# Kernel tuning notes

Hardware: AMD Instinct MI355X
Metric: run time of the kernel (lower is better)

The kernel has to match this reference:

```python
import jax, jax.numpy as jnp
import numpy as np

V, E, R, D, OUT, B = 50000, 400000, 400, 100, 200, 1024
EPS = 1e-5


def ccorr(a, b):
    # circular correlation: irfft(conj(rfft(a)) * rfft(b), n=D)
    return jnp.fft.irfft(jnp.conj(jnp.fft.rfft(a)) * jnp.fft.rfft(b), n=a.shape[-1]).astype(a.dtype)


def setup_inputs() -> dict:
    key = jax.random.key(0)
    ks = jax.random.split(key, 16)
    xav = lambda k, shp: jax.random.normal(k, shp, dtype=jnp.float32) * np.sqrt(2.0 / (shp[0] + shp[-1])) * np.sqrt(2.0)
    return {
        # graph / query (int constants)
        "edge_src": jax.random.randint(ks[0], (E,), 0, V, dtype=jnp.int32),
        "edge_dst": jax.random.randint(ks[1], (E,), 0, V, dtype=jnp.int32),
        "edge_type": jax.random.randint(ks[2], (E,), 0, R, dtype=jnp.int32),
        "head": jax.random.randint(ks[3], (B,), 0, V, dtype=jnp.int32),
        "rela": jax.random.randint(ks[4], (B,), 0, R, dtype=jnp.int32),
        "edge_norm": jax.random.uniform(ks[5], (E,), dtype=jnp.float32),
        # learned parameters
        "ent_emb": xav(ks[6], (V, D)),
        "rel_emb": xav(ks[7], (R, D)),
        "in_w": xav(ks[8], (D, OUT)),
        "out_w": xav(ks[9], (D, OUT)),
        "loop_w": xav(ks[10], (D, OUT)),
        "w_rel": xav(ks[11], (D, OUT)),
        "loop_rel": xav(ks[12], (1, D)),
        "conv_bias": jnp.zeros((OUT,), jnp.float32),
        "bn_gamma": jnp.ones((OUT,), jnp.float32),
        "bn_beta": jnp.zeros((OUT,), jnp.float32),
        "emb_ent": xav(ks[13], (V, OUT)),
        "ent_bias": jnp.zeros((V,), jnp.float32),
    }


def reference(edge_src, edge_dst, edge_type, head, rela, edge_norm,
              ent_emb, rel_emb, in_w, out_w, loop_w, w_rel, loop_rel,
              conv_bias, bn_gamma, bn_beta, emb_ent, ent_bias):
    # --- CompGCNCov (eval mode: dropouts are identity) ---
    h_src = ent_emb[edge_src]          # [E, D] gather
    r_e = rel_emb[edge_type]           # [E, D] gather
    edge_data = ccorr(h_src, r_e)      # [E, D] FFT compose (opn='corr')
    half = E // 2
    msg = jnp.concatenate([edge_data[:half] @ in_w, edge_data[half:] @ out_w])  # [E, OUT]
    msg = msg * edge_norm[:, None]
    agg = jax.ops.segment_sum(msg, edge_dst, num_segments=V) / 3.0             # scatter-sum + /3
    loop = ccorr(ent_emb, jnp.broadcast_to(loop_rel, ent_emb.shape)) @ loop_w / 3.0
    x = agg + loop + conv_bias
    # BatchNorm1d with batch statistics (training-mode stats, affine)
    mean = x.mean(axis=0)
    var = x.var(axis=0)
    x = (x - mean) / jnp.sqrt(var + EPS) * bn_gamma + bn_beta
    x = jnp.tanh(x)                    # act
    r_out = rel_emb @ w_rel            # [R, OUT]
    # --- DistMult decoder ---
    head_emb = x[head]                 # [B, OUT]
    rela_emb = r_out[rela]             # [B, OUT]
    obj = head_emb * rela_emb
    score = jax.nn.sigmoid(obj @ emb_ent.T + ent_bias)  # [B, V]
    return score
```

## Files before the change

### kernel.cpp

```cpp
#include <hip/hip_runtime.h>
#include <cstddef>

constexpr int V = 50000, E = 400000, R = 400, D = 100, OUT = 200, B = 1024;
constexpr int HALF = E / 2;
constexpr float EPS = 1e-5f;
constexpr int K2 = 232;
constexpr int VPAD = 50176;
constexpr int NKEY = 800;
constexpr int E1MAX = 450560;
constexpr int MT_O = 208, MT_K = 128;
constexpr int MT_SZ = MT_O * MT_K;
constexpr int NB2 = 196;
constexpr int BCAP = 2560;
constexpr int ECHK = 4;

typedef short bf16x8 __attribute__((ext_vector_type(8)));
typedef float f32x4  __attribute__((ext_vector_type(4)));
typedef unsigned short ushort8 __attribute__((ext_vector_type(8)));
typedef __attribute__((address_space(1))) const unsigned int guint_t;
typedef __attribute__((address_space(3))) unsigned int luint_t;

__device__ inline unsigned short f2bf(float x) {
    unsigned u = __float_as_uint(x);
    u = (u + 0x7fffu + ((u >> 16) & 1u)) >> 16;
    return (unsigned short)u;
}
__device__ inline float bf2f(unsigned short u) {
    return __uint_as_float(((unsigned)u) << 16);
}

__global__ __launch_bounds__(256) void k_mloop(const float* __restrict__ loop_rel,
                                               const float* __restrict__ loop_w,
                                               float* __restrict__ Mloop) {
    int i = blockIdx.x * 256 + threadIdx.x;
    if (i >= D * OUT) return;
    int j = i / OUT, o = i % OUT;
    float s = 0.f;
    for (int k = 0; k < D; ++k) {
        int idx = j + k; if (idx >= D) idx -= D;
        s += loop_rel[idx] * loop_w[k * OUT + o];
    }
    Mloop[i] = s;
}

__global__ __launch_bounds__(256) void k_rout(const float* __restrict__ rel_emb,
                                              const float* __restrict__ w_rel,
                                              float* __restrict__ r_out) {
    int i = blockIdx.x * 256 + threadIdx.x;
    if (i >= R * OUT) return;
    int r = i / OUT, o = i % OUT;
    float s = 0.f;
    for (int k = 0; k < D; ++k) s += rel_emb[r * D + k] * w_rel[k * OUT + o];
    r_out[i] = s;
}

__global__ __launch_bounds__(256) void k_hist(const int* __restrict__ etyp,
                                              int* __restrict__ hist1) {
    __shared__ int lh[NKEY];
    int t = threadIdx.x;
    for (int i = t; i < NKEY; i += 256) lh[i] = 0;
    __syncthreads();
    for (int e = blockIdx.x * 256 + t; e < E; e += gridDim.x * 256) {
        int key = etyp[e] + (e < HALF ? 0 : R);
        atomicAdd(&lh[key], 1);
    }
    __syncthreads();
    for (int i = t; i < NKEY; i += 256) {
        int c = lh[i];
        if (c) atomicAdd(&hist1[i], c);
    }
}

__global__ __launch_bounds__(1024) void k_scan(const int* __restrict__ hist1,
                                               int* __restrict__ start1,
                                               int* __restrict__ Edev) {
    __shared__ int buf[1024];
    int t = threadIdx.x;
    int c = (t < NKEY) ? ((hist1[t] + 63) & ~63) : 0;
    buf[t] = c; __syncthreads();
    for (int off = 1; off < 1024; off <<= 1) {
        int x = (t >= off) ? buf[t - off] : 0; __syncthreads();
        buf[t] += x; __syncthreads();
    }
    if (t < NKEY) start1[t] = buf[t] - c;
    if (t == NKEY - 1) { start1[NKEY] = buf[t]; *Edev = buf[t]; }
}

__global__ __launch_bounds__(1024) void k_binkey(const int* __restrict__ etyp,
                                                 const int* __restrict__ start1,
                                                 int* __restrict__ cursor1,
                                                 unsigned* __restrict__ perm1,
                                                 int* __restrict__ pos_of_e) {
    __shared__ int lhist[NKEY], lbase[NKEY], lcnt[NKEY];
    int t = threadIdx.x;
    int e0 = blockIdx.x * 8192;
    for (int i = t; i < NKEY; i += 1024) { lhist[i] = 0; lcnt[i] = 0; }
    __syncthreads();
    for (int i = t; i < 8192; i += 1024) {
        int e = e0 + i;
        if (e < E) {
            int key = etyp[e] + (e < HALF ? 0 : R);
            atomicAdd(&lhist[key], 1);
        }
    }
    __syncthreads();
    for (int i = t; i < NKEY; i += 1024) {
        int c = lhist[i];
        lbase[i] = c ? (start1[i] + atomicAdd(&cursor1[i], c)) : 0;
    }
    __syncthreads();
    for (int i = t; i < 8192; i += 1024) {
        int e = e0 + i;
        if (e < E) {
            int key = etyp[e] + (e < HALF ? 0 : R);
            int r = atomicAdd(&lcnt[key], 1);
            int p = lbase[key] + r;
            perm1[p] = (unsigned)e | ((unsigned)key << 19);
            pos_of_e[e] = p;
        }
    }
}

__global__ __launch_bounds__(1024) void k_bindst1(const int* __restrict__ edst,
                                                  const int* __restrict__ pos_of_e,
                                                  int* __restrict__ cursor196,
                                                  uint2* __restrict__ pairs) {
    __shared__ int chist[NB2], cbase[NB2], ccnt[NB2];
    int t = threadIdx.x;
    int e0 = blockIdx.x * 8192;
    for (int i = t; i < NB2; i += 1024) { chist[i] = 0; ccnt[i] = 0; }
    __syncthreads();
    for (int i = t; i < 8192; i += 1024) {
        int e = e0 + i;
        if (e < E) atomicAdd(&chist[edst[e] >> 8], 1);
    }
    __syncthreads();
    for (int i = t; i < NB2; i += 1024) {
        int c = chist[i];
        cbase[i] = c ? atomicAdd(&cursor196[i], c) : 0;
    }
    __syncthreads();
    for (int i = t; i < 8192; i += 1024) {
        int e = e0 + i;
        if (e < E) {
            int d = edst[e];
            int ld = d >> 8;
            int r = atomicAdd(&ccnt[ld], 1);
            int slot = cbase[ld] + r;
            if (slot < BCAP)
                pairs[(size_t)ld * BCAP + slot] = make_uint2((unsigned)d, (unsigned)pos_of_e[e]);
        }
    }
}

__global__ void k_scan2(const int* __restrict__ cursor196,
                        int* __restrict__ bbase, int* __restrict__ start2) {
    __shared__ int buf[256];
    int t = threadIdx.x;
    int c = (t < NB2) ? min(cursor196[t], BCAP) : 0;
    buf[t] = c; __syncthreads();
    for (int off = 1; off < 256; off <<= 1) {
        int x = (t >= off) ? buf[t - off] : 0; __syncthreads();
        buf[t] += x; __syncthreads();
    }
    if (t < NB2) bbase[t] = buf[t] - c;
    if (t == NB2 - 1) { bbase[NB2] = buf[t]; start2[V] = buf[t]; }
}

__global__ __launch_bounds__(256) void k_bindst2(const int* __restrict__ cursor196,
                                                 const int* __restrict__ bbase,
                                                 const uint2* __restrict__ pairs,
                                                 int* __restrict__ start2,
                                                 int* __restrict__ poslist) {
    __shared__ int lcnt[256], loff[256], lrk[256];
    int b = blockIdx.x, t = threadIdx.x;
    lcnt[t] = 0; lrk[t] = 0;
    __syncthreads();
    int n = min(cursor196[b], BCAP);
    int base = bbase[b];
    for (int i = t; i < n; i += 256) {
        int d = (int)pairs[(size_t)b * BCAP + i].x;
        atomicAdd(&lcnt[d - (b << 8)], 1);
    }
    __syncthreads();
    int c = lcnt[t];
    loff[t] = c; __syncthreads();
    for (int off = 1; off < 256; off <<= 1) {
        int x = (t >= off) ? loff[t - off] : 0; __syncthreads();
        loff[t] += x; __syncthreads();
    }
    int excl = loff[t] - c;
    loff[t] = excl;
    int d = (b << 8) + t;
    if (d < V) start2[d] = base + excl;
    __syncthreads();
    for (int i = t; i < n; i += 256) {
        uint2 pr = pairs[(size_t)b * BCAP + i];
        int ld = (int)pr.x - (b << 8);
        int r = atomicAdd(&lrk[ld], 1);
        poslist[base + loff[ld] + r] = (int)pr.y;
    }
}

__global__ __launch_bounds__(256) void k_cvt_ent(const float* __restrict__ ent_emb,
                                                 unsigned short* __restrict__ ent_bf) {
    int i = blockIdx.x * 256 + threadIdx.x;
    if (i >= V * 16) return;
    int v = i >> 4, c8 = i & 15;
    int c0 = c8 * 8;
    ushort8 o = (ushort8)0;
    if (c0 < 96) {
        float4 f0 = *(const float4*)&ent_emb[(size_t)v * D + c0];
        float4 f1 = *(const float4*)&ent_emb[(size_t)v * D + c0 + 4];
        o[0] = f2bf(f0.x); o[1] = f2bf(f0.y); o[2] = f2bf(f0.z); o[3] = f2bf(f0.w);
        o[4] = f2bf(f1.x); o[5] = f2bf(f1.y); o[6] = f2bf(f1.z); o[7] = f2bf(f1.w);
    } else if (c0 == 96) {
        float4 f0 = *(const float4*)&ent_emb[(size_t)v * D + 96];
        o[0] = f2bf(f0.x); o[1] = f2bf(f0.y); o[2] = f2bf(f0.z); o[3] = f2bf(f0.w);
    }
    *(ushort8*)&ent_bf[(size_t)v * 128 + c0] = o;
}

__global__ __launch_bounds__(256) void k_cvt_wt(const float* __restrict__ in_w,
                                                const float* __restrict__ out_w,
                                                unsigned short* __restrict__ WT_bf) {
    int i = blockIdx.x * 256 + threadIdx.x;
    if (i >= 2 * 208 * 16) return;
    int side = i / (208 * 16);
    int rem = i - side * 208 * 16;
    int o = rem >> 4, c8 = rem & 15;
    int k0 = c8 * 8;
    const float* __restrict__ W = side ? out_w : in_w;
    ushort8 v = (ushort8)0;
    if (o < 200) {
#pragma unroll
        for (int q = 0; q < 8; ++q) {
            int k = k0 + q;
            if (k < 100) v[q] = f2bf(W[k * OUT + o]);
        }
    }
    *(ushort8*)&WT_bf[((size_t)side * 208 + o) * 128 + k0] = v;
}

__global__ __launch_bounds__(256) void k_mtab(const float* __restrict__ rel_emb,
                                              const unsigned short* __restrict__ WT_bf,
                                              unsigned short* __restrict__ Mtab) {
    __shared__ unsigned short rsh[256];
    int key = blockIdx.x;
    int rho = (key < R) ? key : key - R;
    int side = (key < R) ? 0 : 1;
    int t = threadIdx.x, lane = t & 63, wid = t >> 6;
    {
        int sm = t;
        if (sm >= 200) sm -= 200; else if (sm >= 100) sm -= 100;
        rsh[t] = f2bf(rel_emb[rho * D + sm]);
    }
    __syncthreads();
    const unsigned short* WT = WT_bf + (size_t)side * 208 * 128;
    unsigned short* MtK = Mtab + (size_t)key * MT_SZ;
    int m16 = lane & 15, kq = lane >> 4;
    for (int jt = 0; jt < 2; ++jt) {
        int j0 = (wid * 2 + jt) * 16;
        f32x4 acc[13] = {};
        for (int ks = 0; ks < 4; ++ks) {
            int rbase = ks * 32 + kq * 8 + j0 + m16;
            ushort8 tmp;
#pragma unroll
            for (int q = 0; q < 8; ++q) tmp[q] = rsh[rbase + q];
            bf16x8 bfr = *(bf16x8*)&tmp;
#pragma unroll
            for (int of = 0; of < 13; ++of) {
                bf16x8 afr = *(const bf16x8*)&WT[(size_t)(of * 16 + m16) * 128 + ks * 32 + kq * 8];
                acc[of] = __builtin_amdgcn_mfma_f32_16x16x32_bf16(afr, bfr, acc[of], 0, 0, 0);
            }
        }
#pragma unroll
        for (int of = 0; of < 13; ++of) {
            int orow = of * 16 + kq * 4;
#pragma unroll
            for (int q = 0; q < 4; ++q)
                MtK[(size_t)(orow + q) * MT_K + j0 + m16] = f2bf(acc[of][q]);
        }
    }
}

__global__ __launch_bounds__(256, 2) void k_edgemm(const unsigned* __restrict__ perm1,
                                                   const int* __restrict__ Edev,
                                                   const int* __restrict__ esrc,
                                                   const float* __restrict__ enorm,
                                                   const unsigned short* __restrict__ ent_bf,
                                                   const unsigned short* __restrict__ Mtab,
                                                   unsigned short* __restrict__ msg) {
    __shared__ __align__(16) unsigned short MtL[MT_SZ];
    __shared__ __align__(16) unsigned short AtL[64 * MT_K];
    __shared__ float snrm[2][64];
    __shared__ int ssrc[2][64];
    int t = threadIdx.x, lane = t & 63, wid = t >> 6;
    int cpx = gridDim.x >> 3;
    int blk = (blockIdx.x & 7) * cpx + (blockIdx.x >> 3);
    int nE = *Edev;
    int curkey = -1;
    for (int c = 0; c < ECHK; ++c) {
        int chunk = blk * ECHK + c;
        if (chunk * 64 >= nE) break;
        int buf = c & 1;
        if (t < 64) {
            unsigned val = perm1[chunk * 64 + t];
            int e = (int)(val & 0x7FFFFu);
            bool ok = (val != 0xFFFFFFFFu);
            ssrc[buf][t] = ok ? esrc[e] : 0;
            snrm[buf][t] = ok ? enorm[e] : 0.f;
        }
        int key = (int)(perm1[chunk * 64] >> 19);
        __syncthreads();
        if (key != curkey) {
            for (int i = 0; i < 13; ++i) {
                int G0 = (wid * 13 + i) * 64;
                int G = G0 + lane;
                int o = G >> 4, g = G & 15;
                int gs = g ^ (o & 7);
                __builtin_amdgcn_global_load_lds(
                    (guint_t*)(Mtab + (size_t)key * MT_SZ + o * MT_K + gs * 8),
                    (luint_t*)(MtL + (size_t)G0 * 8), 16, 0, 0);
            }
            curkey = key;
        }
        for (int i = 0; i < 4; ++i) {
            int base = (wid * 4 + i) * 1024;
            int Gb = base + lane * 16;
            int row = Gb >> 8;
            int g = (Gb >> 4) & 15;
            int gs = g ^ (row & 7);
            __builtin_amdgcn_global_load_lds(
                (guint_t*)(ent_bf + (size_t)ssrc[buf][row] * 128 + gs * 8),
                (luint_t*)((char*)AtL + base), 16, 0, 0);
        }
        __syncthreads();
        int erow = wid * 16 + (lane & 15);
        int kq = lane >> 4;
        f32x4 acc[13] = {};
        for (int ks = 0; ks < 4; ++ks) {
            int g = ks * 4 + kq;
            bf16x8 bfr = *(const bf16x8*)((const char*)AtL + erow * 256 + ((g ^ (erow & 7)) * 16));
#pragma unroll
            for (int of = 0; of < 13; ++of) {
                int orow = of * 16 + (lane & 15);
                bf16x8 afr = *(const bf16x8*)((const char*)MtL + orow * 256 + ((g ^ (orow & 7)) * 16));
                acc[of] = __builtin_amdgcn_mfma_f32_16x16x32_bf16(afr, bfr, acc[of], 0, 0, 0);
            }
        }
        float nr = snrm[buf][erow];
        size_t rowbase = (size_t)(chunk * 64 + erow) * OUT;
#pragma unroll
        for (int of = 0; of < 13; ++of) {
            int o0 = of * 16 + kq * 4;
            if (o0 < OUT) {
                ushort4 pk;
                pk.x = f2bf(acc[of][0] * nr); pk.y = f2bf(acc[of][1] * nr);
                pk.z = f2bf(acc[of][2] * nr); pk.w = f2bf(acc[of][3] * nr);
                *(ushort4*)&msg[rowbase + o0] = pk;
            }
        }
    }
}

__global__ __launch_bounds__(256) void k_agg(const int* __restrict__ start2,
                                             const int* __restrict__ poslist,
                                             const unsigned short* __restrict__ msg,
                                             float* __restrict__ agg) {
    int wid = threadIdx.x >> 6, lane = threadIdx.x & 63;
    int v = blockIdx.x * 4 + wid;
    if (v >= V) return;
    int s = start2[v], epos = start2[v + 1];
    int half = (lane >= 25 && lane < 50) ? 1 : 0;
    int c = lane - half * 25;
    bool act = lane < 50;
    float acc[8] = {};
    for (int q = s; q < epos; q += 2) {
        int qq = q + half;
        if (act && qq < epos) {
            int p = poslist[qq];
            ushort8 m = *(const ushort8*)&msg[(size_t)p * OUT + c * 8];
#pragma unroll
            for (int i = 0; i < 8; ++i) acc[i] += bf2f(m[i]);
        }
    }
    int src = lane + 25 < 64 ? lane + 25 : 63;
#pragma unroll
    for (int i = 0; i < 8; ++i) {
        float o = __shfl(acc[i], src);
        if (lane < 25) acc[i] += o;
    }
    if (lane < 25) {
        float4 o0 = {acc[0], acc[1], acc[2], acc[3]};
        float4 o1 = {acc[4], acc[5], acc[6], acc[7]};
        *(float4*)&agg[(size_t)v * OUT + lane * 8] = o0;
        *(float4*)&agg[(size_t)v * OUT + lane * 8 + 4] = o1;
    }
}

__global__ __launch_bounds__(256) void k_x2(const float* __restrict__ ent_emb,
                                            const float* __restrict__ Mloop,
                                            const float* __restrict__ conv_bias,
                                            float* __restrict__ x) {
    __shared__ float sat[100][36];
    int t = threadIdx.x;
    int v0 = blockIdx.x * 32;
    for (int i = t; i < 800; i += 256) {
        int kg = i >> 5, vv = i & 31;
        int vsafe = min(v0 + vv, V - 1);
        float4 a4 = *(const float4*)&ent_emb[(size_t)vsafe * D + kg * 4];
        sat[kg * 4 + 0][vv] = a4.x;
        sat[kg * 4 + 1][vv] = a4.y;
        sat[kg * 4 + 2][vv] = a4.z;
        sat[kg * 4 + 3][vv] = a4.w;
    }
    __syncthreads();
    if (t < 200) {
        int og = t % 50, eg = t / 50;
        int o0 = og * 4, vv0 = eg * 8;
        float acc[8][4] = {};
        for (int k = 0; k < D; ++k) {
            float4 w4 = *(const float4*)&Mloop[k * OUT + o0];
            float4 ca = *(const float4*)&sat[k][vv0];
            float4 cb = *(const float4*)&sat[k][vv0 + 4];
            float cc[8] = {ca.x, ca.y, ca.z, ca.w, cb.x, cb.y, cb.z, cb.w};
            float wv[4] = {w4.x, w4.y, w4.z, w4.w};
#pragma unroll
            for (int ee = 0; ee < 8; ++ee)
#pragma unroll
                for (int j = 0; j < 4; ++j) acc[ee][j] += cc[ee] * wv[j];
        }
        float4 bi = *(const float4*)&conv_bias[o0];
        float bv[4] = {bi.x, bi.y, bi.z, bi.w};
#pragma unroll
        for (int ee = 0; ee < 8; ++ee) {
            int v = v0 + vv0 + ee;
            if (v < V) {
                size_t base = (size_t)v * OUT + o0;
                float4 ag = *(const float4*)&x[base];
                float4 ov;
                ov.x = (ag.x + acc[ee][0]) * (1.f / 3.f) + bv[0];
                ov.y = (ag.y + acc[ee][1]) * (1.f / 3.f) + bv[1];
                ov.z = (ag.z + acc[ee][2]) * (1.f / 3.f) + bv[2];
                ov.w = (ag.w + acc[ee][3]) * (1.f / 3.f) + bv[3];
                *(float4*)&x[base] = ov;
            }
        }
    }
}

__global__ __launch_bounds__(256) void k_stats(const float* __restrict__ x,
                                               float* __restrict__ colsum,
                                               float* __restrict__ colsq) {
    int g = blockIdx.x * 256 + threadIdx.x;
    int col = g % OUT;
    int r0 = g / OUT;
    float s = 0.f, sq = 0.f;
    for (int r = r0; r < V; r += 512) {
        float v = x[(size_t)r * OUT + col];
        s += v;
        sq += v * v;
    }
    atomicAdd(&colsum[col], s);
    atomicAdd(&colsq[col], sq);
}

__global__ void k_finstats(const float* __restrict__ colsum, const float* __restrict__ colsq,
                           float* __restrict__ mean, float* __restrict__ rstd) {
    int o = threadIdx.x;
    if (o >= OUT) return;
    float m = colsum[o] / (float)V;
    float var = colsq[o] / (float)V - m * m;
    mean[o] = m;
    rstd[o] = rsqrtf(var + EPS);
}

__global__ __launch_bounds__(256) void k_obj(const int* __restrict__ head,
                                             const int* __restrict__ rela,
                                             const float* __restrict__ x,
                                             const float* __restrict__ mean,
                                             const float* __restrict__ rstd,
                                             const float* __restrict__ gamma,
                                             const float* __restrict__ beta,
                                             const float* __restrict__ r_out,
                                             unsigned short* __restrict__ obj_bf) {
    int b = blockIdx.x, t = threadIdx.x;
    if (t >= K2) return;
    float v = 0.f;
    if (t < OUT) {
        int h = head[b], r = rela[b];
        float val = (x[(size_t)h * OUT + t] - mean[t]) * rstd[t] * gamma[t] + beta[t];
        val = tanhf(val);
        v = val * r_out[r * OUT + t];
    }
    obj_bf[(size_t)b * K2 + t] = f2bf(v);
}

__global__ __launch_bounds__(256) void k_cvt_emb(const float* __restrict__ emb_ent,
                                                 unsigned short* __restrict__ emb_bf) {
    int i = blockIdx.x * 256 + threadIdx.x;
    if (i >= VPAD * 29) return;
    int v = i / 29, c8 = i % 29;
    int c0 = c8 * 8;
    ushort8 o = (ushort8)0;
    if (v < V && c0 < 200) {
        float4 f0 = *(const float4*)&emb_ent[(size_t)v * OUT + c0];
        float4 f1 = *(const float4*)&emb_ent[(size_t)v * OUT + c0 + 4];
        o[0] = f2bf(f0.x); o[1] = f2bf(f0.y); o[2] = f2bf(f0.z); o[3] = f2bf(f0.w);
        o[4] = f2bf(f1.x); o[5] = f2bf(f1.y); o[6] = f2bf(f1.z); o[7] = f2bf(f1.w);
    }
    *(ushort8*)&emb_bf[(size_t)v * K2 + c0] = o;
}

constexpr int DEC_BM = 64, DEC_BN = 256;
constexpr int DEC_GX = B / DEC_BM;
constexpr int DEC_GY = VPAD / DEC_BN;
constexpr int DEC_NWG = DEC_GX * DEC_GY;

__global__ __launch_bounds__(256) void k_dec2(const unsigned short* __restrict__ obj_bf,
                                              const unsigned short* __restrict__ emb_bf,
                                              const float* __restrict__ ent_bias,
                                              float* __restrict__ score) {
    int t = threadIdx.x;
    int lane = t & 63, wid = t >> 6;
    int wg = (blockIdx.x & 7) * (DEC_NWG >> 3) + (blockIdx.x >> 3);
    int b0 = (wg & (DEC_GX - 1)) * DEC_BM;
    int v0 = (wg >> 4) * DEC_BN;
    int r16 = lane & 15;
    int kc = (lane >> 4) * 8;
    int vbase = v0 + wid * 64;
    const unsigned short* gA = obj_bf + (size_t)(b0 + r16) * K2 + kc;
    const unsigned short* gB = emb_bf + (size_t)(vbase + r16) * K2 + kc;
    f32x4 acc[4][4] = {};
    for (int ks = 0; ks < 7; ++ks) {
        int kof = ks * 32;
        bf16x8 a[4], bb[4];
#pragma unroll
        for (int mf = 0; mf < 4; ++mf)
            a[mf] = *(const bf16x8*)(gA + (size_t)(mf * 16) * K2 + kof);
#pragma unroll
        for (int nf = 0; nf < 4; ++nf)
            bb[nf] = *(const bf16x8*)(gB + (size_t)(nf * 16) * K2 + kof);
#pragma unroll
        for (int mf = 0; mf < 4; ++mf)
#pragma unroll
            for (int nf = 0; nf < 4; ++nf)
                acc[mf][nf] = __builtin_amdgcn_mfma_f32_16x16x32_bf16(a[mf], bb[nf],
                                                                      acc[mf][nf], 0, 0, 0);
    }
#pragma unroll
    for (int nf = 0; nf < 4; ++nf) {
        int v = vbase + nf * 16 + r16;
        if (v >= V) continue;
        float bias = ent_bias[v];
#pragma unroll
        for (int mf = 0; mf < 4; ++mf) {
            int brow = b0 + mf * 16 + (lane >> 4) * 4;
            f32x4 av = acc[mf][nf];
#pragma unroll
            for (int i = 0; i < 4; ++i) {
                float val = av[i] + bias;
                score[(size_t)(brow + i) * V + v] = 1.f / (1.f + __expf(-val));
            }
        }
    }
}

extern "C" void kernel_launch(void* const* d_in, const int* in_sizes, int n_in,
                              void* d_out, int out_size, void* d_ws, size_t ws_size,
                              hipStream_t stream) {
    const int*   edge_src  = (const int*)d_in[0];
    const int*   edge_dst  = (const int*)d_in[1];
    const int*   edge_type = (const int*)d_in[2];
    const int*   head      = (const int*)d_in[3];
    const int*   rela      = (const int*)d_in[4];
    const float* edge_norm = (const float*)d_in[5];
    const float* ent_emb   = (const float*)d_in[6];
    const float* rel_emb   = (const float*)d_in[7];
    const float* in_w      = (const float*)d_in[8];
    const float* out_w     = (const float*)d_in[9];
    const float* loop_w    = (const float*)d_in[10];
    const float* w_rel     = (const float*)d_in[11];
    const float* loop_rel  = (const float*)d_in[12];
    const float* conv_bias = (const float*)d_in[13];
    const float* bn_gamma  = (const float*)d_in[14];
    const float* bn_beta   = (const float*)d_in[15];
    const float* emb_ent   = (const float*)d_in[16];
    const float* ent_bias  = (const float*)d_in[17];
    float* score = (float*)d_out;

    char* w = (char*)d_ws;
    float*          agg    = (float*)w;                      w += (size_t)V * OUT * 4;
    unsigned short* Mtab   = (unsigned short*)w;             w += (size_t)NKEY * MT_SZ * 2;
    unsigned*       perm1  = (unsigned*)w;                   w += (size_t)E1MAX * 4;
    int*            pos_of_e = (int*)w;                      w += (size_t)E * 4;
    int*            poslist  = (int*)w;                      w += (size_t)E * 4;
    uint2*          pairs    = (uint2*)w;                    w += (size_t)NB2 * BCAP * 8;
    char* zbase = w;
    int*   hist1     = (int*)w;                              w += NKEY * 4;
    int*   cursor1   = (int*)w;                              w += NKEY * 4;
    int*   cursor196 = (int*)w;                              w += NB2 * 4;
    float* colsum    = (float*)w;                            w += OUT * 4;
    float* colsq     = (float*)w;                            w += OUT * 4;
    size_t zbytes = (size_t)(w - zbase);
    int*   start1  = (int*)w;                                w += (NKEY + 1) * 4;
    int*   start2  = (int*)w;                                w += (V + 4) * 4;
    int*   bbase   = (int*)w;                                w += (NB2 + 4) * 4;
    int*   Edev    = (int*)w;                                w += 16;
    float* meanp   = (float*)w;                              w += OUT * 4;
    float* rstdp   = (float*)w;                              w += OUT * 4;
    float* Mloop   = (float*)w;                              w += (size_t)D * OUT * 4;
    float* r_out   = (float*)w;                              w += (size_t)R * OUT * 4;
    unsigned short* obj_bf = (unsigned short*)w;             w += (size_t)B * K2 * 2;
    unsigned short* WT_bf  = (unsigned short*)w;             w += (size_t)2 * 208 * 128 * 2;
    unsigned short* ent_bf = (unsigned short*)agg;
    unsigned short* emb_bf = (unsigned short*)agg;
    unsigned short* msg    = (unsigned short*)d_out;

    hipMemsetAsync(zbase, 0, zbytes, stream);
    hipMemsetAsync(perm1, 0xFF, (size_t)E1MAX * 4, stream);

    k_hist<<<512, 256, 0, stream>>>(edge_type, hist1);
    k_scan<<<1, 1024, 0, stream>>>(hist1, start1, Edev);
    k_binkey<<<(E + 8191) / 8192, 1024, 0, stream>>>(edge_type, start1, cursor1,
                                                     perm1, pos_of_e);
    k_bindst1<<<(E + 8191) / 8192, 1024, 0, stream>>>(edge_dst, pos_of_e, cursor196, pairs);
    k_scan2<<<1, 256, 0, stream>>>(cursor196, bbase, start2);
    k_bindst2<<<NB2, 256, 0, stream>>>(cursor196, bbase, pairs, start2, poslist);
    k_cvt_wt<<<(2 * 208 * 16 + 255) / 256, 256, 0, stream>>>(in_w, out_w, WT_bf);
    k_mtab<<<NKEY, 256, 0, stream>>>(rel_emb, WT_bf, Mtab);
    k_mloop<<<(D * OUT + 255) / 256, 256, 0, stream>>>(loop_rel, loop_w, Mloop);
    k_rout<<<(R * OUT + 255) / 256, 256, 0, stream>>>(rel_emb, w_rel, r_out);
    k_cvt_ent<<<(V * 16 + 255) / 256, 256, 0, stream>>>(ent_emb, ent_bf);
    k_edgemm<<<E1MAX / 64 / ECHK, 256, 0, stream>>>(perm1, Edev, edge_src, edge_norm,
                                                    ent_bf, Mtab, msg);
    k_agg<<<V / 4, 256, 0, stream>>>(start2, poslist, msg, agg);
    k_x2<<<(V + 31) / 32, 256, 0, stream>>>(ent_emb, Mloop, conv_bias, agg);
    k_stats<<<400, 256, 0, stream>>>(agg, colsum, colsq);
    k_finstats<<<1, 256, 0, stream>>>(colsum, colsq, meanp, rstdp);
    k_obj<<<B, 256, 0, stream>>>(head, rela, agg, meanp, rstdp, bn_gamma, bn_beta,
                                 r_out, obj_bf);
    k_cvt_emb<<<(VPAD * 29 + 255) / 256, 256, 0, stream>>>(emb_ent, emb_bf);
    k_dec2<<<DEC_NWG, 256, 0, stream>>>(obj_bf, emb_bf, ent_bias, score);
}
```

Baseline: 441.8 us.

## Fuse small preprocessing kernels, merge aggregation with self-loop, inline scans and stats

Combines the mloop, rout, weight-convert and entity-convert kernels into one launch, folds the second-level bin scan into k_bindst2, and computes BN mean/rstd inside k_obj. It also fuses the neighbour aggregation with the self-loop GEMM, so the aggregate stays in shared memory instead of being written and reread through global memory. ECHK is doubled so each edge-GEMM workgroup handles more chunks. The aim is fewer launches and less global traffic, at the cost of redundant per-block scans and a smaller loop-GEMM tile per block.

```diff
diff --git a/kernel.cpp b/kernel.cpp
--- a/kernel.cpp
+++ b/kernel.cpp
@@ -12,7 +12,7 @@
 constexpr int MT_SZ = MT_O * MT_K;
 constexpr int NB2 = 196;
 constexpr int BCAP = 2560;
-constexpr int ECHK = 4;
+constexpr int ECHK = 8;
 
 typedef short bf16x8 __attribute__((ext_vector_type(8)));
 typedef float f32x4  __attribute__((ext_vector_type(4)));
@@ -29,29 +29,77 @@
     return __uint_as_float(((unsigned)u) << 16);
 }
 
-__global__ __launch_bounds__(256) void k_mloop(const float* __restrict__ loop_rel,
-                                               const float* __restrict__ loop_w,
-                                               float* __restrict__ Mloop) {
-    int i = blockIdx.x * 256 + threadIdx.x;
-    if (i >= D * OUT) return;
-    int j = i / OUT, o = i % OUT;
-    float s = 0.f;
-    for (int k = 0; k < D; ++k) {
-        int idx = j + k; if (idx >= D) idx -= D;
-        s += loop_rel[idx] * loop_w[k * OUT + o];
-    }
-    Mloop[i] = s;
-}
-
-__global__ __launch_bounds__(256) void k_rout(const float* __restrict__ rel_emb,
-                                              const float* __restrict__ w_rel,
-                                              float* __restrict__ r_out) {
-    int i = blockIdx.x * 256 + threadIdx.x;
-    if (i >= R * OUT) return;
-    int r = i / OUT, o = i % OUT;
-    float s = 0.f;
-    for (int k = 0; k < D; ++k) s += rel_emb[r * D + k] * w_rel[k * OUT + o];
-    r_out[i] = s;
+constexpr int G_MLOOP = (D * OUT + 255) / 256;
+constexpr int G_ROUT  = (R * OUT + 255) / 256;
+constexpr int G_CVTWT = (2 * 208 * 16) / 256;
+constexpr int G_CVTENT = (V * 16) / 256;
+constexpr int PRE_B1 = G_MLOOP;
+constexpr int PRE_B2 = PRE_B1 + G_ROUT;
+constexpr int PRE_B3 = PRE_B2 + G_CVTWT;
+constexpr int PRE_NWG = PRE_B3 + G_CVTENT;
+
+__global__ __launch_bounds__(256) void k_pre(const float* __restrict__ loop_rel,
+                                             const float* __restrict__ loop_w,
+                                             const float* __restrict__ rel_emb,
+                                             const float* __restrict__ w_rel,
+                                             const float* __restrict__ in_w,
+                                             const float* __restrict__ out_w,
+                                             const float* __restrict__ ent_emb,
+                                             float* __restrict__ Mloop,
+                                             float* __restrict__ r_out,
+                                             unsigned short* __restrict__ WT_bf,
+                                             unsigned short* __restrict__ ent_bf) {
+    int blk = blockIdx.x, t = threadIdx.x;
+    if (blk < PRE_B1) {
+        int i = blk * 256 + t;
+        if (i >= D * OUT) return;
+        int j = i / OUT, o = i % OUT;
+        float s = 0.f;
+        for (int k = 0; k < D; ++k) {
+            int idx = j + k; if (idx >= D) idx -= D;
+            s += loop_rel[idx] * loop_w[k * OUT + o];
+        }
+        Mloop[i] = s;
+    } else if (blk < PRE_B2) {
+        int i = (blk - PRE_B1) * 256 + t;
+        if (i >= R * OUT) return;
+        int r = i / OUT, o = i % OUT;
+        float s = 0.f;
+        for (int k = 0; k < D; ++k) s += rel_emb[r * D + k] * w_rel[k * OUT + o];
+        r_out[i] = s;
+    } else if (blk < PRE_B3) {
+        int i = (blk - PRE_B2) * 256 + t;
+        int side = i / (208 * 16);
+        int rem = i - side * 208 * 16;
+        int o = rem >> 4, c8 = rem & 15;
+        int k0 = c8 * 8;
+        const float* __restrict__ W = side ? out_w : in_w;
+        ushort8 v = (ushort8)0;
+        if (o < 200) {
+#pragma unroll
+            for (int q = 0; q < 8; ++q) {
+                int k = k0 + q;
+                if (k < 100) v[q] = f2bf(W[k * OUT + o]);
+            }
+        }
+        *(ushort8*)&WT_bf[((size_t)side * 208 + o) * 128 + k0] = v;
+    } else {
+        int i = (blk - PRE_B3) * 256 + t;
+        if (i >= V * 16) return;
+        int v = i >> 4, c8 = i & 15;
+        int c0 = c8 * 8;
+        ushort8 o = (ushort8)0;
+        if (c0 < 96) {
+            float4 f0 = *(const float4*)&ent_emb[(size_t)v * D + c0];
+            float4 f1 = *(const float4*)&ent_emb[(size_t)v * D + c0 + 4];
+            o[0] = f2bf(f0.x); o[1] = f2bf(f0.y); o[2] = f2bf(f0.z); o[3] = f2bf(f0.w);
+            o[4] = f2bf(f1.x); o[5] = f2bf(f1.y); o[6] = f2bf(f1.z); o[7] = f2bf(f1.w);
+        } else if (c0 == 96) {
+            float4 f0 = *(const float4*)&ent_emb[(size_t)v * D + 96];
+            o[0] = f2bf(f0.x); o[1] = f2bf(f0.y); o[2] = f2bf(f0.z); o[3] = f2bf(f0.w);
+        }
+        *(ushort8*)&ent_bf[(size_t)v * 128 + c0] = o;
+    }
 }
 
 __global__ __launch_bounds__(256) void k_hist(const int* __restrict__ etyp,
@@ -153,43 +201,34 @@
     }
 }
 
-__global__ void k_scan2(const int* __restrict__ cursor196,
-                        int* __restrict__ bbase, int* __restrict__ start2) {
-    __shared__ int buf[256];
-    int t = threadIdx.x;
-    int c = (t < NB2) ? min(cursor196[t], BCAP) : 0;
-    buf[t] = c; __syncthreads();
-    for (int off = 1; off < 256; off <<= 1) {
-        int x = (t >= off) ? buf[t - off] : 0; __syncthreads();
-        buf[t] += x; __syncthreads();
-    }
-    if (t < NB2) bbase[t] = buf[t] - c;
-    if (t == NB2 - 1) { bbase[NB2] = buf[t]; start2[V] = buf[t]; }
-}
-
 __global__ __launch_bounds__(256) void k_bindst2(const int* __restrict__ cursor196,
-                                                 const int* __restrict__ bbase,
                                                  const uint2* __restrict__ pairs,
                                                  int* __restrict__ start2,
                                                  int* __restrict__ poslist) {
-    __shared__ int lcnt[256], loff[256], lrk[256];
+    __shared__ int lcnt[256], loff[256], lrk[256], bscan[256];
     int b = blockIdx.x, t = threadIdx.x;
     lcnt[t] = 0; lrk[t] = 0;
-    __syncthreads();
+    bscan[t] = (t < NB2) ? min(cursor196[t], BCAP) : 0;
+    __syncthreads();
+    for (int off = 1; off < 256; off <<= 1) {
+        int xx = (t >= off) ? bscan[t - off] : 0; __syncthreads();
+        bscan[t] += xx; __syncthreads();
+    }
+    int base = (b > 0) ? bscan[b - 1] : 0;
+    if (b == 0 && t == 0) start2[V] = bscan[NB2 - 1];
     int n = min(cursor196[b], BCAP);
-    int base = bbase[b];
     for (int i = t; i < n; i += 256) {
         int d = (int)pairs[(size_t)b * BCAP + i].x;
         atomicAdd(&lcnt[d - (b << 8)], 1);
     }
     __syncthreads();
-    int c = lcnt[t];
-    loff[t] = c; __syncthreads();
+    int cc = lcnt[t];
+    loff[t] = cc; __syncthreads();
     for (int off = 1; off < 256; off <<= 1) {
-        int x = (t >= off) ? loff[t - off] : 0; __syncthreads();
-        loff[t] += x; __syncthreads();
-    }
-    int excl = loff[t] - c;
+        int xx = (t >= off) ? loff[t - off] : 0; __syncthreads();
+        loff[t] += xx; __syncthreads();
+    }
+    int excl = loff[t] - cc;
     loff[t] = excl;
     int d = (b << 8) + t;
     if (d < V) start2[d] = base + excl;
@@ -200,46 +239,6 @@
         int r = atomicAdd(&lrk[ld], 1);
         poslist[base + loff[ld] + r] = (int)pr.y;
     }
-}
-
-__global__ __launch_bounds__(256) void k_cvt_ent(const float* __restrict__ ent_emb,
-                                                 unsigned short* __restrict__ ent_bf) {
-    int i = blockIdx.x * 256 + threadIdx.x;
-    if (i >= V * 16) return;
-    int v = i >> 4, c8 = i & 15;
-    int c0 = c8 * 8;
-    ushort8 o = (ushort8)0;
-    if (c0 < 96) {
-        float4 f0 = *(const float4*)&ent_emb[(size_t)v * D + c0];
-        float4 f1 = *(const float4*)&ent_emb[(size_t)v * D + c0 + 4];
-        o[0] = f2bf(f0.x); o[1] = f2bf(f0.y); o[2] = f2bf(f0.z); o[3] = f2bf(f0.w);
-        o[4] = f2bf(f1.x); o[5] = f2bf(f1.y); o[6] = f2bf(f1.z); o[7] = f2bf(f1.w);
-    } else if (c0 == 96) {
-        float4 f0 = *(const float4*)&ent_emb[(size_t)v * D + 96];
-        o[0] = f2bf(f0.x); o[1] = f2bf(f0.y); o[2] = f2bf(f0.z); o[3] = f2bf(f0.w);
-    }
-    *(ushort8*)&ent_bf[(size_t)v * 128 + c0] = o;
-}
-
-__global__ __launch_bounds__(256) void k_cvt_wt(const float* __restrict__ in_w,
-                                                const float* __restrict__ out_w,
-                                                unsigned short* __restrict__ WT_bf) {
-    int i = blockIdx.x * 256 + threadIdx.x;
-    if (i >= 2 * 208 * 16) return;
-    int side = i / (208 * 16);
-    int rem = i - side * 208 * 16;
-    int o = rem >> 4, c8 = rem & 15;
-    int k0 = c8 * 8;
-    const float* __restrict__ W = side ? out_w : in_w;
-    ushort8 v = (ushort8)0;
-    if (o < 200) {
-#pragma unroll
-        for (int q = 0; q < 8; ++q) {
-            int k = k0 + q;
-            if (k < 100) v[q] = f2bf(W[k * OUT + o]);
-        }
-    }
-    *(ushort8*)&WT_bf[((size_t)side * 208 + o) * 128 + k0] = v;
 }
 
 __global__ __launch_bounds__(256) void k_mtab(const float* __restrict__ rel_emb,
@@ -364,52 +363,47 @@
     }
 }
 
-__global__ __launch_bounds__(256) void k_agg(const int* __restrict__ start2,
-                                             const int* __restrict__ poslist,
-                                             const unsigned short* __restrict__ msg,
-                                             float* __restrict__ agg) {
-    int wid = threadIdx.x >> 6, lane = threadIdx.x & 63;
-    int v = blockIdx.x * 4 + wid;
-    if (v >= V) return;
-    int s = start2[v], epos = start2[v + 1];
+__global__ __launch_bounds__(256) void k_aggx(const int* __restrict__ start2,
+                                              const int* __restrict__ poslist,
+                                              const unsigned short* __restrict__ msg,
+                                              const float* __restrict__ ent_emb,
+                                              const float* __restrict__ Mloop,
+                                              const float* __restrict__ conv_bias,
+                                              float* __restrict__ x) {
+    __shared__ float xt[16][200];
+    __shared__ float sat[100][20];
+    int t = threadIdx.x, lane = t & 63, wid = t >> 6;
+    int v0 = blockIdx.x * 16;
     int half = (lane >= 25 && lane < 50) ? 1 : 0;
     int c = lane - half * 25;
     bool act = lane < 50;
-    float acc[8] = {};
-    for (int q = s; q < epos; q += 2) {
-        int qq = q + half;
-        if (act && qq < epos) {
-            int p = poslist[qq];
-            ushort8 m = *(const ushort8*)&msg[(size_t)p * OUT + c * 8];
-#pragma unroll
-            for (int i = 0; i < 8; ++i) acc[i] += bf2f(m[i]);
-        }
-    }
     int src = lane + 25 < 64 ? lane + 25 : 63;
-#pragma unroll
-    for (int i = 0; i < 8; ++i) {
-        float o = __shfl(acc[i], src);
-        if (lane < 25) acc[i] += o;
-    }
-    if (lane < 25) {
-        float4 o0 = {acc[0], acc[1], acc[2], acc[3]};
-        float4 o1 = {acc[4], acc[5], acc[6], acc[7]};
-        *(float4*)&agg[(size_t)v * OUT + lane * 8] = o0;
-        *(float4*)&agg[(size_t)v * OUT + lane * 8 + 4] = o1;
-    }
-}
-
-__global__ __launch_bounds__(256) void k_x2(const float* __restrict__ ent_emb,
-                                            const float* __restrict__ Mloop,
-                                            const float* __restrict__ conv_bias,
-                                            float* __restrict__ x) {
-    __shared__ float sat[100][36];
-    int t = threadIdx.x;
-    int v0 = blockIdx.x * 32;
-    for (int i = t; i < 800; i += 256) {
-        int kg = i >> 5, vv = i & 31;
-        int vsafe = min(v0 + vv, V - 1);
-        float4 a4 = *(const float4*)&ent_emb[(size_t)vsafe * D + kg * 4];
+    for (int i = 0; i < 4; ++i) {
+        int v = v0 + wid * 4 + i;
+        int s = start2[v], epos = start2[v + 1];
+        float acc[8] = {};
+        for (int q = s; q < epos; q += 2) {
+            int qq = q + half;
+            if (act && qq < epos) {
+                int p = poslist[qq];
+                ushort8 m = *(const ushort8*)&msg[(size_t)p * OUT + c * 8];
+#pragma unroll
+                for (int j = 0; j < 8; ++j) acc[j] += bf2f(m[j]);
+            }
+        }
+#pragma unroll
+        for (int j = 0; j < 8; ++j) {
+            float o = __shfl(acc[j], src);
+            if (lane < 25) acc[j] += o;
+        }
+        if (lane < 25) {
+#pragma unroll
+            for (int j = 0; j < 8; ++j) xt[wid * 4 + i][lane * 8 + j] = acc[j];
+        }
+    }
+    for (int i = t; i < 400; i += 256) {
+        int kg = i >> 4, vv = i & 15;
+        float4 a4 = *(const float4*)&ent_emb[(size_t)(v0 + vv) * D + kg * 4];
         sat[kg * 4 + 0][vv] = a4.x;
         sat[kg * 4 + 1][vv] = a4.y;
         sat[kg * 4 + 2][vv] = a4.z;
@@ -418,34 +412,29 @@
     __syncthreads();
     if (t < 200) {
         int og = t % 50, eg = t / 50;
-        int o0 = og * 4, vv0 = eg * 8;
-        float acc[8][4] = {};
+        int o0 = og * 4, vv0 = eg * 4;
+        float acc[4][4] = {};
         for (int k = 0; k < D; ++k) {
             float4 w4 = *(const float4*)&Mloop[k * OUT + o0];
             float4 ca = *(const float4*)&sat[k][vv0];
-            float4 cb = *(const float4*)&sat[k][vv0 + 4];
-            float cc[8] = {ca.x, ca.y, ca.z, ca.w, cb.x, cb.y, cb.z, cb.w};
+            float cc[4] = {ca.x, ca.y, ca.z, ca.w};
             float wv[4] = {w4.x, w4.y, w4.z, w4.w};
 #pragma unroll
-            for (int ee = 0; ee < 8; ++ee)
-#pragma unroll
-                for (int j = 0; j < 4; ++j) acc[ee][j] += cc[ee] * wv[j];
+            for (int r = 0; r < 4; ++r)
+#pragma unroll
+                for (int j = 0; j < 4; ++j) acc[r][j] += cc[r] * wv[j];
         }
         float4 bi = *(const float4*)&conv_bias[o0];
         float bv[4] = {bi.x, bi.y, bi.z, bi.w};
 #pragma unroll
-        for (int ee = 0; ee < 8; ++ee) {
-            int v = v0 + vv0 + ee;
-            if (v < V) {
-                size_t base = (size_t)v * OUT + o0;
-                float4 ag = *(const float4*)&x[base];
-                float4 ov;
-                ov.x = (ag.x + acc[ee][0]) * (1.f / 3.f) + bv[0];
-                ov.y = (ag.y + acc[ee][1]) * (1.f / 3.f) + bv[1];
-                ov.z = (ag.z + acc[ee][2]) * (1.f / 3.f) + bv[2];
-                ov.w = (ag.w + acc[ee][3]) * (1.f / 3.f) + bv[3];
-                *(float4*)&x[base] = ov;
-            }
+        for (int r = 0; r < 4; ++r) {
+            int vv = vv0 + r;
+            float4 ov;
+            ov.x = (xt[vv][o0 + 0] + acc[r][0]) * (1.f / 3.f) + bv[0];
+            ov.y = (xt[vv][o0 + 1] + acc[r][1]) * (1.f / 3.f) + bv[1];
+            ov.z = (xt[vv][o0 + 2] + acc[r][2]) * (1.f / 3.f) + bv[2];
+            ov.w = (xt[vv][o0 + 3] + acc[r][3]) * (1.f / 3.f) + bv[3];
+            *(float4*)&x[(size_t)(v0 + vv) * OUT + o0] = ov;
         }
     }
 }
@@ -466,21 +455,11 @@
     atomicAdd(&colsq[col], sq);
 }
 
-__global__ void k_finstats(const float* __restrict__ colsum, const float* __restrict__ colsq,
-                           float* __restrict__ mean, float* __restrict__ rstd) {
-    int o = threadIdx.x;
-    if (o >= OUT) return;
-    float m = colsum[o] / (float)V;
-    float var = colsq[o] / (float)V - m * m;
-    mean[o] = m;
-    rstd[o] = rsqrtf(var + EPS);
-}
-
 __global__ __launch_bounds__(256) void k_obj(const int* __restrict__ head,
                                              const int* __restrict__ rela,
                                              const float* __restrict__ x,
-                                             const float* __restrict__ mean,
-                                             const float* __restrict__ rstd,
+                                             const float* __restrict__ colsum,
+                                             const float* __restrict__ colsq,
                                              const float* __restrict__ gamma,
                                              const float* __restrict__ beta,
                                              const float* __restrict__ r_out,
@@ -489,8 +468,11 @@
     if (t >= K2) return;
     float v = 0.f;
     if (t < OUT) {
+        float m = colsum[t] / (float)V;
+        float var = colsq[t] / (float)V - m * m;
+        float rs = rsqrtf(var + EPS);
         int h = head[b], r = rela[b];
-        float val = (x[(size_t)h * OUT + t] - mean[t]) * rstd[t] * gamma[t] + beta[t];
+        float val = (x[(size_t)h * OUT + t] - m) * rs * gamma[t] + beta[t];
         val = tanhf(val);
         v = val * r_out[r * OUT + t];
     }
@@ -606,10 +588,7 @@
     size_t zbytes = (size_t)(w - zbase);
     int*   start1  = (int*)w;                                w += (NKEY + 1) * 4;
     int*   start2  = (int*)w;                                w += (V + 4) * 4;
-    int*   bbase   = (int*)w;                                w += (NB2 + 4) * 4;
     int*   Edev    = (int*)w;                                w += 16;
-    float* meanp   = (float*)w;                              w += OUT * 4;
-    float* rstdp   = (float*)w;                              w += OUT * 4;
     float* Mloop   = (float*)w;                              w += (size_t)D * OUT * 4;
     float* r_out   = (float*)w;                              w += (size_t)R * OUT * 4;
     unsigned short* obj_bf = (unsigned short*)w;             w += (size_t)B * K2 * 2;
@@ -626,20 +605,16 @@
     k_binkey<<<(E + 8191) / 8192, 1024, 0, stream>>>(edge_type, start1, cursor1,
                                                      perm1, pos_of_e);
     k_bindst1<<<(E + 8191) / 8192, 1024, 0, stream>>>(edge_dst, pos_of_e, cursor196, pairs);
-    k_scan2<<<1, 256, 0, stream>>>(cursor196, bbase, start2);
-    k_bindst2<<<NB2, 256, 0, stream>>>(cursor196, bbase, pairs, start2, poslist);
-    k_cvt_wt<<<(2 * 208 * 16 + 255) / 256, 256, 0, stream>>>(in_w, out_w, WT_bf);
+    k_bindst2<<<NB2, 256, 0, stream>>>(cursor196, pairs, start2, poslist);
+    k_pre<<<PRE_NWG, 256, 0, stream>>>(loop_rel, loop_w, rel_emb, w_rel, in_w, out_w,
+                                       ent_emb, Mloop, r_out, WT_bf, ent_bf);
     k_mtab<<<NKEY, 256, 0, stream>>>(rel_emb, WT_bf, Mtab);
-    k_mloop<<<(D * OUT + 255) / 256, 256, 0, stream>>>(loop_rel, loop_w, Mloop);
-    k_rout<<<(R * OUT + 255) / 256, 256, 0, stream>>>(rel_emb, w_rel, r_out);
-    k_cvt_ent<<<(V * 16 + 255) / 256, 256, 0, stream>>>(ent_emb, ent_bf);
     k_edgemm<<<E1MAX / 64 / ECHK, 256, 0, stream>>>(perm1, Edev, edge_src, edge_norm,
                                                     ent_bf, Mtab, msg);
-    k_agg<<<V / 4, 256, 0, stream>>>(start2, poslist, msg, agg);
-    k_x2<<<(V + 31) / 32, 256, 0, stream>>>(ent_emb, Mloop, conv_bias, agg);
+    k_aggx<<<V / 16, 256, 0, stream>>>(start2, poslist, msg, ent_emb, Mloop,
+                                       conv_bias, agg);
     k_stats<<<400, 256, 0, stream>>>(agg, colsum, colsq);
-    k_finstats<<<1, 256, 0, stream>>>(colsum, colsq, meanp, rstdp);
-    k_obj<<<B, 256, 0, stream>>>(head, rela, agg, meanp, rstdp, bn_gamma, bn_beta,
+    k_obj<<<B, 256, 0, stream>>>(head, rela, agg, colsum, colsq, bn_gamma, bn_beta,
                                  r_out, obj_bf);
     k_cvt_emb<<<(VPAD * 29 + 255) / 256, 256, 0, stream>>>(emb_ent, emb_bf);
     k_dec2<<<DEC_NWG, 256, 0, stream>>>(obj_bf, emb_bf, ent_bias, score);
```

Measured after the change: 413.7 us. 6.4% less time.
